# Kernel tuning notes

Hardware: AMD Instinct MI355X
Metric: run time of the kernel (lower is better)

The kernel has to match this reference:

```python
import math
import jax, jax.numpy as jnp
import numpy as np

N, T, C, C2, H, W = 4, 8, 256, 256, 32, 32


def setup_inputs() -> dict:
    key = jax.random.key(0)
    k1, k2, k3 = jax.random.split(key, 3)
    return {
        "key": jax.random.normal(k1, (N, T, C, H, W), dtype=jnp.float32),
        "query": jax.random.normal(k2, (N, T, C, H, W), dtype=jnp.float32),
        "value": jax.random.normal(k3, (N, T, C2, H, W), dtype=jnp.float32),
    }


def reference(key, query, value):
    n, t, c, h, w = key.shape
    c2 = value.shape[2]
    hw = h * w
    k = key.reshape(n, t, c, hw)      # (n,t,c,p)
    q = query.reshape(n, t, c, hw)    # (n,t,c,q)
    v = value.reshape(n, t, c2, hw)   # (n,t,c2,p)
    # scores[p,q] = sum_c K[c,p] * Q[c,q], scaled by sqrt(c)
    scores = jnp.einsum("ntcp,ntcq->ntpq", k, q) / math.sqrt(c)
    # non-standard: softmax over the KEY axis (dim=-2)
    p_attn = jax.nn.softmax(scores, axis=-2)
    # non-standard: V @ attn (contract over key positions p)
    p_val = jnp.einsum("ntcp,ntpq->ntcq", v, p_attn).reshape(n, t, c2, h, w)
    return p_val, p_attn.reshape(n, t, h, w, h, w)
```

## Files before the change

### kernel.cpp

```cpp
#include <hip/hip_runtime.h>
#include <hip/hip_bf16.h>


#define NT_BATCH 32
#define CDIM     256
#define HW       1024

using short8 = __attribute__((ext_vector_type(8))) short;
using f32x16 = __attribute__((ext_vector_type(16))) float;
using f32x4v = __attribute__((ext_vector_type(4))) float;

__device__ __forceinline__ unsigned pk2(float a, float b) {
  float2 t; t.x = a; t.y = b;
  __hip_bfloat162 h = __float22bfloat162_rn(t);
  return *reinterpret_cast<unsigned*>(&h);
}
__device__ __forceinline__ void wr64(void* dst, float a, float b, float c, float d) {
  uint2 v; v.x = pk2(a, b); v.y = pk2(c, d);
  *reinterpret_cast<uint2*>(dst) = v;
}

__device__ __forceinline__ void barrier_lgkm() {
  __builtin_amdgcn_sched_barrier(0);
  asm volatile("s_waitcnt lgkmcnt(0)" ::: "memory");
  __builtin_amdgcn_s_barrier();
  __builtin_amdgcn_sched_barrier(0);
}

union SMEM {
  struct { unsigned short Qs[64][264]; unsigned short As[256][72]; } a;
  struct { unsigned short Vs[256][72]; unsigned short Ps[64][72]; } b;
};

__global__ __launch_bounds__(512, 4) void k_fused(const float* __restrict__ Kp,
                                                  const float* __restrict__ Qp,
                                                  const float* __restrict__ Vp,
                                                  float* __restrict__ A_out,
                                                  float* __restrict__ O) {
  __shared__ __align__(16) SMEM sm;
  __shared__ float csum[64];
  __shared__ float inv_s[64];

  const int hbid = blockIdx.y * 16 + blockIdx.x;
  const int lbid = ((hbid & 7) << 6) | (hbid >> 3);
  const int nt = lbid >> 4;
  const int q0 = (lbid & 15) << 6;

  const float* Kb = Kp + (size_t)nt * (CDIM * HW);
  const float* Qb = Qp + (size_t)nt * (CDIM * HW);
  const float* Vb = Vp + (size_t)nt * (CDIM * HW);
  float* Ab = A_out + (size_t)nt * (HW * HW);
  float* Ob = O + (size_t)nt * (CDIM * HW);

  const int t = threadIdx.x, lane = t & 63;
  const int wave = t >> 6;
  const int l31 = lane & 31, lhi = lane >> 5;

  if (t < 64) csum[t] = 0.f;

  #pragma unroll
  for (int j2 = 0; j2 < 2; ++j2) {
    const int u = t + (j2 << 9);
    const int cb4 = (u & 63) << 2, qb4 = (u >> 6) << 2;
    f32x4v qv[4];
    #pragma unroll
    for (int j = 0; j < 4; ++j)
      qv[j] = *(const f32x4v*)&Qb[(size_t)(cb4 + j) * HW + q0 + qb4];
    #pragma unroll
    for (int i = 0; i < 4; ++i)
      wr64(&sm.a.Qs[qb4 + i][cb4], qv[0][i], qv[1][i], qv[2][i], qv[3][i]);
  }

  f32x4v kreg[2][4];
  auto loadK = [&](int P0_, int C0_) {
    #pragma unroll
    for (int j2 = 0; j2 < 2; ++j2) {
      const int u = t + (j2 << 9);
      const int cb = (u & 15) << 2, pp = (u >> 4) << 2;
      #pragma unroll
      for (int j = 0; j < 4; ++j)
        kreg[j2][j] = *(const f32x4v*)&Kb[(size_t)(C0_ + cb + j) * HW + P0_ + pp];
    }
  };

  float part[2] = {0.f, 0.f};
  loadK(0, 0);
  #pragma unroll
  for (int pt = 0; pt < 4; ++pt) {
    const int P0 = pt << 8;
    f32x16 acc[2];
    #pragma unroll
    for (int n = 0; n < 2; ++n)
      #pragma unroll
      for (int r = 0; r < 16; ++r) acc[n][r] = 0.f;

    #pragma unroll
    for (int cc = 0; cc < 4; ++cc) {
      barrier_lgkm();
      #pragma unroll
      for (int j2 = 0; j2 < 2; ++j2) {
        const int u = t + (j2 << 9);
        const int cb = (u & 15) << 2, pp = (u >> 4) << 2;
        #pragma unroll
        for (int i = 0; i < 4; ++i)
          wr64(&sm.a.As[pp + i][cb],
               kreg[j2][0][i], kreg[j2][1][i], kreg[j2][2][i], kreg[j2][3][i]);
      }
      if (cc < 3) loadK(P0, (cc + 1) << 6);
      else if (pt < 3) loadK(P0 + 256, 0);
      barrier_lgkm();
      __builtin_amdgcn_s_setprio(1);
      #pragma unroll
      for (int ks = 0; ks < 4; ++ks) {
        short8 a_ = *(const short8*)&sm.a.As[wave * 32 + l31][ks * 16 + lhi * 8];
        short8 b0 = *(const short8*)&sm.a.Qs[l31][(cc << 6) + ks * 16 + lhi * 8];
        short8 b1 = *(const short8*)&sm.a.Qs[32 + l31][(cc << 6) + ks * 16 + lhi * 8];
        acc[0] = __builtin_amdgcn_mfma_f32_32x32x16_bf16(a_, b0, acc[0], 0, 0, 0);
        acc[1] = __builtin_amdgcn_mfma_f32_32x32x16_bf16(a_, b1, acc[1], 0, 0, 0);
      }
      __builtin_amdgcn_s_setprio(0);
    }

    const int rbase = wave * 32 + (lhi << 2);
    #pragma unroll
    for (int n = 0; n < 2; ++n) {
      const int col = q0 + n * 32 + l31;
      #pragma unroll
      for (int r = 0; r < 16; ++r) {
        float e = __expf(acc[n][r] * 0.0625f);
        part[n] += e;
        const int row = P0 + rbase + (r & 3) + ((r >> 2) << 3);
        Ab[(size_t)row * HW + col] = e;
      }
    }
  }

  atomicAdd(&csum[l31], part[0]);
  atomicAdd(&csum[32 + l31], part[1]);
  __syncthreads();
  if (t < 64) inv_s[t] = 1.0f / csum[t];
  __syncthreads();

  const int pr2 = t >> 4;
  const int sq = (t & 15) << 2;
  const f32x4v inv4 = *(const f32x4v*)&inv_s[sq];
  const int vc = t >> 1, vp = (t & 1) << 5;

  f32x4v er[2][2];
  f32x4v vreg[8];
  auto loadE = [&](int buf, int pb_) {
    er[buf][0] = *(const f32x4v*)&Ab[(size_t)(pb_ + 2 * pr2) * HW + q0 + sq];
    er[buf][1] = *(const f32x4v*)&Ab[(size_t)(pb_ + 2 * pr2 + 1) * HW + q0 + sq];
  };
  auto loadV = [&](int pb_) {
    #pragma unroll
    for (int g = 0; g < 8; ++g)
      vreg[g] = *(const f32x4v*)&Vb[(size_t)vc * HW + pb_ + vp + (g << 2)];
  };

  f32x16 av[2];
  #pragma unroll
  for (int n = 0; n < 2; ++n)
    #pragma unroll
    for (int r = 0; r < 16; ++r) av[n][r] = 0.f;

  loadE(0, 0); loadV(0); loadE(1, 64);
  #pragma unroll
  for (int tile = 0; tile < 16; ++tile) {
    const int pb = tile << 6;
    const int cur = tile & 1;
    const f32x4v a0 = er[cur][0] * inv4;
    const f32x4v a1 = er[cur][1] * inv4;
    barrier_lgkm();
    #pragma unroll
    for (int j = 0; j < 4; ++j)
      *reinterpret_cast<unsigned*>(&sm.b.Ps[sq + j][2 * pr2]) = pk2(a0[j], a1[j]);
    #pragma unroll
    for (int g = 0; g < 4; ++g) {
      uint4 w_;
      w_.x = pk2(vreg[2 * g][0], vreg[2 * g][1]);
      w_.y = pk2(vreg[2 * g][2], vreg[2 * g][3]);
      w_.z = pk2(vreg[2 * g + 1][0], vreg[2 * g + 1][1]);
      w_.w = pk2(vreg[2 * g + 1][2], vreg[2 * g + 1][3]);
      *reinterpret_cast<uint4*>(&sm.b.Vs[vc][vp + (g << 3)]) = w_;
    }
    if (tile < 15) loadV(pb + 64);
    if (tile < 14) loadE(cur, pb + 128);
    *(f32x4v*)&Ab[(size_t)(pb + 2 * pr2) * HW + q0 + sq] = a0;
    *(f32x4v*)&Ab[(size_t)(pb + 2 * pr2 + 1) * HW + q0 + sq] = a1;
    barrier_lgkm();
    __builtin_amdgcn_s_setprio(1);
    #pragma unroll
    for (int kk = 0; kk < 4; ++kk) {
      short8 a_ = *(const short8*)&sm.b.Vs[wave * 32 + l31][kk * 16 + lhi * 8];
      short8 b0 = *(const short8*)&sm.b.Ps[l31][kk * 16 + lhi * 8];
      short8 b1 = *(const short8*)&sm.b.Ps[32 + l31][kk * 16 + lhi * 8];
      av[0] = __builtin_amdgcn_mfma_f32_32x32x16_bf16(a_, b0, av[0], 0, 0, 0);
      av[1] = __builtin_amdgcn_mfma_f32_32x32x16_bf16(a_, b1, av[1], 0, 0, 0);
    }
    __builtin_amdgcn_s_setprio(0);
  }

  #pragma unroll
  for (int n = 0; n < 2; ++n) {
    const int col = q0 + n * 32 + l31;
    const int cbase = wave * 32 + (lhi << 2);
    #pragma unroll
    for (int r = 0; r < 16; ++r) {
      const int c = cbase + (r & 3) + ((r >> 2) << 3);
      Ob[(size_t)c * HW + col] = av[n][r];
    }
  }
}

extern "C" void kernel_launch(void* const* d_in, const int* in_sizes, int n_in,
                              void* d_out, int out_size, void* d_ws, size_t ws_size,
                              hipStream_t stream) {
  const float* key   = (const float*)d_in[0];
  const float* query = (const float*)d_in[1];
  const float* value = (const float*)d_in[2];
  float* out  = (float*)d_out;
  float* pval = out;
  float* attn = out + (size_t)NT_BATCH * CDIM * HW;

  k_fused<<<dim3(16, NT_BATCH), 512, 0, stream>>>(key, query, value, attn, pval);
}
```

Measured before the change: 406.9 us.

## Fuse PV matmul into score loop using unnormalized exp, normalize afterwards

Folds the P·V product into the score loop: each 256-row score tile is exponentiated, staged to shared memory as bf16 directly from the accumulators, and multiplied with V at once, so the separate PV pass no longer re-reads the exp values from global memory. Normalization moves to the end: the output is scaled by the inverse column sums, and the attention matrix gets one final read-scale-write pass. Q gets its own shared buffer so the K tile and the V/P tiles can share a union, and K and V prefetches reuse one register array. The cost is more barriers inside the score loop and, as in the code before, no max subtraction before the exponent.

```diff
diff --git a/kernel.cpp b/kernel.cpp
--- a/kernel.cpp
+++ b/kernel.cpp
@@ -18,6 +18,11 @@
 __device__ __forceinline__ void wr64(void* dst, float a, float b, float c, float d) {
   uint2 v; v.x = pk2(a, b); v.y = pk2(c, d);
   *reinterpret_cast<uint2*>(dst) = v;
+}
+__device__ __forceinline__ void wr128(void* dst, f32x4v p0, f32x4v p1) {
+  uint4 v; v.x = pk2(p0[0], p0[1]); v.y = pk2(p0[2], p0[3]);
+  v.z = pk2(p1[0], p1[1]); v.w = pk2(p1[2], p1[3]);
+  *reinterpret_cast<uint4*>(dst) = v;
 }
 
 __device__ __forceinline__ void barrier_lgkm() {
@@ -28,8 +33,8 @@
 }
 
 union SMEM {
-  struct { unsigned short Qs[64][264]; unsigned short As[256][72]; } a;
-  struct { unsigned short Vs[256][72]; unsigned short Ps[64][72]; } b;
+  unsigned short As[256][72];
+  struct { unsigned short Vs[256][72]; unsigned short Ps[64][72]; } pv;
 };
 
 __global__ __launch_bounds__(512, 4) void k_fused(const float* __restrict__ Kp,
@@ -37,6 +42,7 @@
                                                   const float* __restrict__ Vp,
                                                   float* __restrict__ A_out,
                                                   float* __restrict__ O) {
+  __shared__ __align__(16) unsigned short Qs[64][264];
   __shared__ __align__(16) SMEM sm;
   __shared__ float csum[64];
   __shared__ float inv_s[64];
@@ -58,6 +64,25 @@
 
   if (t < 64) csum[t] = 0.f;
 
+  f32x4v pf[8];
+  const int kcb = (t & 15) << 2, kpp = ((t >> 4) << 2) & 255;
+  const int kpp2 = (((t + 512) >> 4) << 2) & 255;
+  auto loadK = [&](int P0_, int C0_) {
+    #pragma unroll
+    for (int j = 0; j < 4; ++j) {
+      pf[j]     = *(const f32x4v*)&Kb[(size_t)(C0_ + kcb + j) * HW + P0_ + kpp];
+      pf[4 + j] = *(const f32x4v*)&Kb[(size_t)(C0_ + kcb + j) * HW + P0_ + kpp2];
+    }
+  };
+  const int vc = t >> 1, vp = (t & 1) << 5;
+  auto loadV = [&](int p0_) {
+    #pragma unroll
+    for (int g = 0; g < 8; ++g)
+      pf[g] = *(const f32x4v*)&Vb[(size_t)vc * HW + p0_ + vp + (g << 2)];
+  };
+
+  loadK(0, 0);
+
   #pragma unroll
   for (int j2 = 0; j2 < 2; ++j2) {
     const int u = t + (j2 << 9);
@@ -68,24 +93,16 @@
       qv[j] = *(const f32x4v*)&Qb[(size_t)(cb4 + j) * HW + q0 + qb4];
     #pragma unroll
     for (int i = 0; i < 4; ++i)
-      wr64(&sm.a.Qs[qb4 + i][cb4], qv[0][i], qv[1][i], qv[2][i], qv[3][i]);
-  }
-
-  f32x4v kreg[2][4];
-  auto loadK = [&](int P0_, int C0_) {
-    #pragma unroll
-    for (int j2 = 0; j2 < 2; ++j2) {
-      const int u = t + (j2 << 9);
-      const int cb = (u & 15) << 2, pp = (u >> 4) << 2;
-      #pragma unroll
-      for (int j = 0; j < 4; ++j)
-        kreg[j2][j] = *(const f32x4v*)&Kb[(size_t)(C0_ + cb + j) * HW + P0_ + pp];
-    }
-  };
+      wr64(&Qs[qb4 + i][cb4], qv[0][i], qv[1][i], qv[2][i], qv[3][i]);
+  }
 
   float part[2] = {0.f, 0.f};
-  loadK(0, 0);
+  f32x16 av[2];
   #pragma unroll
+  for (int n = 0; n < 2; ++n)
+    #pragma unroll
+    for (int r = 0; r < 16; ++r) av[n][r] = 0.f;
+
   for (int pt = 0; pt < 4; ++pt) {
     const int P0 = pt << 8;
     f32x16 acc[2];
@@ -98,23 +115,19 @@
     for (int cc = 0; cc < 4; ++cc) {
       barrier_lgkm();
       #pragma unroll
-      for (int j2 = 0; j2 < 2; ++j2) {
-        const int u = t + (j2 << 9);
-        const int cb = (u & 15) << 2, pp = (u >> 4) << 2;
-        #pragma unroll
-        for (int i = 0; i < 4; ++i)
-          wr64(&sm.a.As[pp + i][cb],
-               kreg[j2][0][i], kreg[j2][1][i], kreg[j2][2][i], kreg[j2][3][i]);
+      for (int i = 0; i < 4; ++i) {
+        wr64(&sm.As[kpp + i][kcb],  pf[0][i], pf[1][i], pf[2][i], pf[3][i]);
+        wr64(&sm.As[kpp2 + i][kcb], pf[4][i], pf[5][i], pf[6][i], pf[7][i]);
       }
       if (cc < 3) loadK(P0, (cc + 1) << 6);
-      else if (pt < 3) loadK(P0 + 256, 0);
+      else        loadV(P0);
       barrier_lgkm();
       __builtin_amdgcn_s_setprio(1);
       #pragma unroll
       for (int ks = 0; ks < 4; ++ks) {
-        short8 a_ = *(const short8*)&sm.a.As[wave * 32 + l31][ks * 16 + lhi * 8];
-        short8 b0 = *(const short8*)&sm.a.Qs[l31][(cc << 6) + ks * 16 + lhi * 8];
-        short8 b1 = *(const short8*)&sm.a.Qs[32 + l31][(cc << 6) + ks * 16 + lhi * 8];
+        short8 a_ = *(const short8*)&sm.As[wave * 32 + l31][ks * 16 + lhi * 8];
+        short8 b0 = *(const short8*)&Qs[l31][(cc << 6) + ks * 16 + lhi * 8];
+        short8 b1 = *(const short8*)&Qs[32 + l31][(cc << 6) + ks * 16 + lhi * 8];
         acc[0] = __builtin_amdgcn_mfma_f32_32x32x16_bf16(a_, b0, acc[0], 0, 0, 0);
         acc[1] = __builtin_amdgcn_mfma_f32_32x32x16_bf16(a_, b1, acc[1], 0, 0, 0);
       }
@@ -127,11 +140,43 @@
       const int col = q0 + n * 32 + l31;
       #pragma unroll
       for (int r = 0; r < 16; ++r) {
-        float e = __expf(acc[n][r] * 0.0625f);
-        part[n] += e;
+        acc[n][r] = __expf(acc[n][r] * 0.0625f);
+        part[n] += acc[n][r];
         const int row = P0 + rbase + (r & 3) + ((r >> 2) << 3);
-        Ab[(size_t)row * HW + col] = e;
-      }
+        Ab[(size_t)row * HW + col] = acc[n][r];
+      }
+    }
+
+    #pragma unroll
+    for (int j = 0; j < 4; ++j) {
+      barrier_lgkm();
+      wr128(&sm.pv.Vs[vc][vp],      pf[0], pf[1]);
+      wr128(&sm.pv.Vs[vc][vp + 8],  pf[2], pf[3]);
+      wr128(&sm.pv.Vs[vc][vp + 16], pf[4], pf[5]);
+      wr128(&sm.pv.Vs[vc][vp + 24], pf[6], pf[7]);
+      if ((wave >> 1) == j) {
+        const int pbase = (wave & 1) * 32 + (lhi << 2);
+        #pragma unroll
+        for (int n = 0; n < 2; ++n)
+          #pragma unroll
+          for (int g = 0; g < 4; ++g)
+            wr64(&sm.pv.Ps[n * 32 + l31][pbase + (g << 3)],
+                 acc[n][4 * g], acc[n][4 * g + 1],
+                 acc[n][4 * g + 2], acc[n][4 * g + 3]);
+      }
+      if (j < 3)      loadV(P0 + ((j + 1) << 6));
+      else if (pt < 3) loadK(P0 + 256, 0);
+      barrier_lgkm();
+      __builtin_amdgcn_s_setprio(1);
+      #pragma unroll
+      for (int kk = 0; kk < 4; ++kk) {
+        short8 a_ = *(const short8*)&sm.pv.Vs[wave * 32 + l31][kk * 16 + lhi * 8];
+        short8 b0 = *(const short8*)&sm.pv.Ps[l31][kk * 16 + lhi * 8];
+        short8 b1 = *(const short8*)&sm.pv.Ps[32 + l31][kk * 16 + lhi * 8];
+        av[0] = __builtin_amdgcn_mfma_f32_32x32x16_bf16(a_, b0, av[0], 0, 0, 0);
+        av[1] = __builtin_amdgcn_mfma_f32_32x32x16_bf16(a_, b1, av[1], 0, 0, 0);
+      }
+      __builtin_amdgcn_s_setprio(0);
     }
   }
 
@@ -141,75 +186,29 @@
   if (t < 64) inv_s[t] = 1.0f / csum[t];
   __syncthreads();
 
-  const int pr2 = t >> 4;
-  const int sq = (t & 15) << 2;
-  const f32x4v inv4 = *(const f32x4v*)&inv_s[sq];
-  const int vc = t >> 1, vp = (t & 1) << 5;
-
-  f32x4v er[2][2];
-  f32x4v vreg[8];
-  auto loadE = [&](int buf, int pb_) {
-    er[buf][0] = *(const f32x4v*)&Ab[(size_t)(pb_ + 2 * pr2) * HW + q0 + sq];
-    er[buf][1] = *(const f32x4v*)&Ab[(size_t)(pb_ + 2 * pr2 + 1) * HW + q0 + sq];
-  };
-  auto loadV = [&](int pb_) {
-    #pragma unroll
-    for (int g = 0; g < 8; ++g)
-      vreg[g] = *(const f32x4v*)&Vb[(size_t)vc * HW + pb_ + vp + (g << 2)];
-  };
-
-  f32x16 av[2];
-  #pragma unroll
-  for (int n = 0; n < 2; ++n)
-    #pragma unroll
-    for (int r = 0; r < 16; ++r) av[n][r] = 0.f;
-
-  loadE(0, 0); loadV(0); loadE(1, 64);
-  #pragma unroll
-  for (int tile = 0; tile < 16; ++tile) {
-    const int pb = tile << 6;
-    const int cur = tile & 1;
-    const f32x4v a0 = er[cur][0] * inv4;
-    const f32x4v a1 = er[cur][1] * inv4;
-    barrier_lgkm();
-    #pragma unroll
-    for (int j = 0; j < 4; ++j)
-      *reinterpret_cast<unsigned*>(&sm.b.Ps[sq + j][2 * pr2]) = pk2(a0[j], a1[j]);
-    #pragma unroll
-    for (int g = 0; g < 4; ++g) {
-      uint4 w_;
-      w_.x = pk2(vreg[2 * g][0], vreg[2 * g][1]);
-      w_.y = pk2(vreg[2 * g][2], vreg[2 * g][3]);
-      w_.z = pk2(vreg[2 * g + 1][0], vreg[2 * g + 1][1]);
-      w_.w = pk2(vreg[2 * g + 1][2], vreg[2 * g + 1][3]);
-      *reinterpret_cast<uint4*>(&sm.b.Vs[vc][vp + (g << 3)]) = w_;
-    }
-    if (tile < 15) loadV(pb + 64);
-    if (tile < 14) loadE(cur, pb + 128);
-    *(f32x4v*)&Ab[(size_t)(pb + 2 * pr2) * HW + q0 + sq] = a0;
-    *(f32x4v*)&Ab[(size_t)(pb + 2 * pr2 + 1) * HW + q0 + sq] = a1;
-    barrier_lgkm();
-    __builtin_amdgcn_s_setprio(1);
-    #pragma unroll
-    for (int kk = 0; kk < 4; ++kk) {
-      short8 a_ = *(const short8*)&sm.b.Vs[wave * 32 + l31][kk * 16 + lhi * 8];
-      short8 b0 = *(const short8*)&sm.b.Ps[l31][kk * 16 + lhi * 8];
-      short8 b1 = *(const short8*)&sm.b.Ps[32 + l31][kk * 16 + lhi * 8];
-      av[0] = __builtin_amdgcn_mfma_f32_32x32x16_bf16(a_, b0, av[0], 0, 0, 0);
-      av[1] = __builtin_amdgcn_mfma_f32_32x32x16_bf16(a_, b1, av[1], 0, 0, 0);
-    }
-    __builtin_amdgcn_s_setprio(0);
-  }
-
   #pragma unroll
   for (int n = 0; n < 2; ++n) {
     const int col = q0 + n * 32 + l31;
+    const float invc = inv_s[n * 32 + l31];
     const int cbase = wave * 32 + (lhi << 2);
     #pragma unroll
     for (int r = 0; r < 16; ++r) {
       const int c = cbase + (r & 3) + ((r >> 2) << 3);
-      Ob[(size_t)c * HW + col] = av[n][r];
-    }
+      Ob[(size_t)c * HW + col] = av[n][r] * invc;
+    }
+  }
+
+  const int trow = t >> 4;
+  const int sq = (t & 15) << 2;
+  const f32x4v inv4 = *(const f32x4v*)&inv_s[sq];
+  for (int s = 0; s < 32; s += 8) {
+    f32x4v er[8];
+    #pragma unroll
+    for (int u = 0; u < 8; ++u)
+      er[u] = *(const f32x4v*)&Ab[(size_t)(((s + u) << 5) + trow) * HW + q0 + sq];
+    #pragma unroll
+    for (int u = 0; u < 8; ++u)
+      *(f32x4v*)&Ab[(size_t)(((s + u) << 5) + trow) * HW + q0 + sq] = er[u] * inv4;
   }
 }
 
```

Measured after the change: 462.7 us. 13.7% more time.
